# Performance work log

Hardware: AMD Instinct MI355X
Metric: run time of the kernel (lower is better)

The kernel has to match this reference:

```python
import jax, jax.numpy as jnp
import numpy as np

B, C, H, W = 256, 3, 224, 224
RETINA = 32
NUM_ZOOM = 3
SCALE = 2
HG, HL = 1024, 256  # num_hidden_glimpse, num_hidden_location
GDIM = NUM_ZOOM * C * RETINA * RETINA  # 9216


def setup_inputs() -> dict:
    key = jax.random.key(0)
    ks = jax.random.split(key, 12)
    images = jax.random.normal(ks[0], (B, C, H, W), dtype=jnp.float32)
    # locations in [-0.4, 0.4] so all multi-scale crops are in-bounds
    locations = (jax.random.uniform(ks[1], (B, 2), dtype=jnp.float32) * 2.0 - 1.0) * 0.4
    def lin(kw, kb, fan_in, fan_out):
        s = 1.0 / np.sqrt(fan_in)
        Wm = jax.random.uniform(kw, (fan_in, fan_out), jnp.float32, -s, s)
        bm = jax.random.uniform(kb, (fan_out,), jnp.float32, -s, s)
        return Wm, bm
    W1, b1 = lin(ks[2], ks[3], GDIM, HG)
    W2, b2 = lin(ks[4], ks[5], 2, HL)
    W3, b3 = lin(ks[6], ks[7], HG, HG + HL)
    W4, b4 = lin(ks[8], ks[9], HL, HG + HL)
    return {"images": images, "locations": locations,
            "W1": W1, "b1": b1, "W2": W2, "b2": b2,
            "W3": W3, "b3": b3, "W4": W4, "b4": b4}


def _foveate(images, locations):
    # images (B,C,H,W); locations (B,2) in [-1,1]
    denorm = (locations + 1.0) * 0.5 * W  # denormalized pixel coords (row, col)
    zoom_patches = []
    for i in range(NUM_ZOOM):
        half = int(RETINA * 0.5 * SCALE ** i)
        size = 2 * half
        def crop(img, loc):
            # int() truncation == floor for in-bounds (non-negative) offsets
            top = jnp.trunc(loc[0] - half).astype(jnp.int32)
            left = jnp.trunc(loc[1] - half).astype(jnp.int32)
            return jax.lax.dynamic_slice(img, (jnp.int32(0), top, left), (C, size, size))
        crops = jax.vmap(crop)(images, denorm)  # (B,C,size,size)
        resized = jax.image.resize(crops, (crops.shape[0], C, RETINA, RETINA),
                                   method="bilinear", antialias=False)
        zoom_patches.append(resized)
    g = jnp.stack(zoom_patches, axis=1)  # (B, Z, C, r, r)
    return g.reshape(g.shape[0], -1)  # (B, Z*C*r*r)


def reference(images, locations, W1, b1, W2, b2, W3, b3, W4, b4):
    g = _foveate(images, locations)
    hg = jax.nn.relu(jax.nn.relu(g @ W1 + b1) @ W3 + b3)
    hl = jax.nn.relu(jax.nn.relu(locations @ W2 + b2) @ W4 + b4)
    return jax.nn.relu(hg + hl)
```

## Files before the change

kernel.cpp:

```cpp
#include <hip/hip_runtime.h>

typedef __attribute__((ext_vector_type(8))) short short8;
typedef __attribute__((ext_vector_type(4))) float f32x4;

#define Bsz 256
#define Cch 3
#define Him 224
#define Wim 224
#define RET 32
#define HG 1024
#define HL 256
#define GDIM 9216
#define NOUT 1280

__device__ __forceinline__ unsigned short f2bf(float x) {
  unsigned u = __float_as_uint(x);
  unsigned r = (u + 0x7fffu + ((u >> 16) & 1u)) >> 16;
  return (unsigned short)r;
}
__device__ __forceinline__ float bf2f(unsigned short h) {
  return __uint_as_float((unsigned)h << 16);
}

__global__ __launch_bounds__(256) void foveate_kernel(
    const float* __restrict__ img, const float* __restrict__ loc,
    unsigned short* __restrict__ ghi, unsigned short* __restrict__ glo) {
  int idx = blockIdx.x * 256 + threadIdx.x;
  int b = idx / GDIM;
  int r = idx - b * GDIM;
  int z = r / (Cch * RET * RET);
  int r2 = r - z * (Cch * RET * RET);
  int c = r2 / (RET * RET);
  int p = r2 - c * (RET * RET);
  int i = p >> 5, j = p & 31;
  float dr = (loc[b * 2 + 0] + 1.f) * .5f * (float)Wim;
  float dc = (loc[b * 2 + 1] + 1.f) * .5f * (float)Wim;
  int half = 16 << z;
  int top = (int)truncf(dr - (float)half), left = (int)truncf(dc - (float)half);
  const float* base = img + ((long)b * Cch + c) * (Him * Wim);
  float v;
  if (z == 0) {
    v = base[(top + i) * Wim + left + j];
  } else {
    int rr = (z == 1) ? top + 2 * i : top + 4 * i + 1;
    int cc = (z == 1) ? left + 2 * j : left + 4 * j + 1;
    v = .25f * (base[rr * Wim + cc] + base[rr * Wim + cc + 1] +
                base[(rr + 1) * Wim + cc] + base[(rr + 1) * Wim + cc + 1]);
  }
  unsigned short h = f2bf(v);
  ghi[idx] = h;
  glo[idx] = f2bf(v - bf2f(h));
}

__global__ __launch_bounds__(256) void tconv_kernel(
    const float* __restrict__ in, unsigned short* __restrict__ oh,
    unsigned short* __restrict__ ol, int K, int N) {
  __shared__ float tile[32][33];
  int n0 = blockIdx.x * 32, k0 = blockIdx.y * 32;
  int r = threadIdx.x >> 3, c4 = (threadIdx.x & 7) * 4;
  float4 v = *(const float4*)(in + (long)(k0 + r) * N + n0 + c4);
  tile[r][c4 + 0] = v.x; tile[r][c4 + 1] = v.y;
  tile[r][c4 + 2] = v.z; tile[r][c4 + 3] = v.w;
  __syncthreads();
  float x0 = tile[c4 + 0][r], x1 = tile[c4 + 1][r];
  float x2 = tile[c4 + 2][r], x3 = tile[c4 + 3][r];
  unsigned short h0 = f2bf(x0), h1 = f2bf(x1), h2 = f2bf(x2), h3 = f2bf(x3);
  long o = (long)(n0 + r) * K + k0 + c4;
  *(ushort4*)(oh + o) = make_ushort4(h0, h1, h2, h3);
  *(ushort4*)(ol + o) = make_ushort4(f2bf(x0 - bf2f(h0)), f2bf(x1 - bf2f(h1)),
                                     f2bf(x2 - bf2f(h2)), f2bf(x3 - bf2f(h3)));
}

__device__ __forceinline__ void mfma_tile(
    const unsigned short* __restrict__ Ahi, const unsigned short* __restrict__ Alo, int lda,
    const unsigned short* __restrict__ Bhi, const unsigned short* __restrict__ Blo, int ldb,
    int m0, int n0, int kb, int iters, f32x4 acc[4][4], unsigned short* lds) {
  const int t = threadIdx.x;
  const int lane = t & 63;
  const int wm = (t >> 7) & 1, wn = (t >> 6) & 1;
  unsigned short* pAh = lds;
  unsigned short* pAl = lds + 4096;
  unsigned short* pBh = lds + 8192;
  unsigned short* pBl = lds + 12288;
  const int c0 = t, c1 = t + 256;
  const int r0 = c0 >> 2, ko0 = c0 & 3;
  const int r1 = c1 >> 2, ko1 = c1 & 3;
  const long a0 = (long)(m0 + r0) * lda + kb + ko0 * 8;
  const long a1 = (long)(m0 + r1) * lda + kb + ko1 * 8;
  const long b0 = (long)(n0 + r0) * ldb + kb + ko0 * 8;
  const long b1 = (long)(n0 + r1) * ldb + kb + ko1 * 8;
  const int d0 = ((r0 >> 4) * 64 + (r0 & 15) + ko0 * 16) * 8;
  const int d1 = ((r1 >> 4) * 64 + (r1 & 15) + ko1 * 16) * 8;

  for (int it = 0; it < iters; ++it) {
    const long ka = (long)it * 32;
    uint4 vah0 = *(const uint4*)(Ahi + a0 + ka);
    uint4 vah1 = *(const uint4*)(Ahi + a1 + ka);
    uint4 val0 = *(const uint4*)(Alo + a0 + ka);
    uint4 val1 = *(const uint4*)(Alo + a1 + ka);
    uint4 vbh0 = *(const uint4*)(Bhi + b0 + ka);
    uint4 vbh1 = *(const uint4*)(Bhi + b1 + ka);
    uint4 vbl0 = *(const uint4*)(Blo + b0 + ka);
    uint4 vbl1 = *(const uint4*)(Blo + b1 + ka);
    __syncthreads();
    *(uint4*)(pAh + d0) = vah0; *(uint4*)(pAh + d1) = vah1;
    *(uint4*)(pAl + d0) = val0; *(uint4*)(pAl + d1) = val1;
    *(uint4*)(pBh + d0) = vbh0; *(uint4*)(pBh + d1) = vbh1;
    *(uint4*)(pBl + d0) = vbl0; *(uint4*)(pBl + d1) = vbl1;
    __syncthreads();
    short8 ah[4], al[4], bh[4], bl[4];
#pragma unroll
    for (int f = 0; f < 4; ++f) {
      int ra = ((wm * 4 + f) * 64 + lane) * 8;
      int rb = ((wn * 4 + f) * 64 + lane) * 8;
      ah[f] = *(const short8*)(pAh + ra);
      al[f] = *(const short8*)(pAl + ra);
      bh[f] = *(const short8*)(pBh + rb);
      bl[f] = *(const short8*)(pBl + rb);
    }
#pragma unroll
    for (int mf = 0; mf < 4; ++mf)
#pragma unroll
      for (int nf = 0; nf < 4; ++nf) {
        acc[mf][nf] = __builtin_amdgcn_mfma_f32_16x16x32_bf16(ah[mf], bh[nf], acc[mf][nf], 0, 0, 0);
        acc[mf][nf] = __builtin_amdgcn_mfma_f32_16x16x32_bf16(ah[mf], bl[nf], acc[mf][nf], 0, 0, 0);
        acc[mf][nf] = __builtin_amdgcn_mfma_f32_16x16x32_bf16(al[mf], bh[nf], acc[mf][nf], 0, 0, 0);
      }
  }
}

__device__ __forceinline__ void epilogue(float* __restrict__ Pz, int ldp, int m0, int n0,
                                         f32x4 acc[4][4]) {
  const int t = threadIdx.x, lane = t & 63;
  const int wm = (t >> 7) & 1, wn = (t >> 6) & 1;
  const int rbase = (lane >> 4) * 4, col = lane & 15;
#pragma unroll
  for (int mf = 0; mf < 4; ++mf)
#pragma unroll
    for (int nf = 0; nf < 4; ++nf) {
      int row = m0 + wm * 64 + mf * 16 + rbase;
      int cc = n0 + wn * 64 + nf * 16 + col;
#pragma unroll
      for (int r = 0; r < 4; ++r)
        Pz[(long)(row + r) * ldp + cc] = acc[mf][nf][r];
    }
}

__global__ __launch_bounds__(256, 2) void gemm1_kernel(
    const unsigned short* __restrict__ ghi, const unsigned short* __restrict__ glo,
    const unsigned short* __restrict__ w1thi, const unsigned short* __restrict__ w1tlo,
    float* __restrict__ P) {
  __shared__ __align__(16) unsigned short lds[16384];
  f32x4 zz = {0.f, 0.f, 0.f, 0.f};
  f32x4 acc[4][4];
  for (int i = 0; i < 4; ++i) for (int j = 0; j < 4; ++j) acc[i][j] = zz;
  int n0 = blockIdx.x * 128, m0 = blockIdx.y * 128, z = blockIdx.z;
  mfma_tile(ghi, glo, GDIM, w1thi, w1tlo, GDIM, m0, n0, z * 288, 9, acc, lds);
  epilogue(P + (long)z * Bsz * HG, HG, m0, n0, acc);
}

__global__ __launch_bounds__(256, 2) void gemm2_kernel(
    const unsigned short* __restrict__ h1hi, const unsigned short* __restrict__ h1lo,
    const unsigned short* __restrict__ h2hi, const unsigned short* __restrict__ h2lo,
    const unsigned short* __restrict__ w3thi, const unsigned short* __restrict__ w3tlo,
    const unsigned short* __restrict__ w4thi, const unsigned short* __restrict__ w4tlo,
    float* __restrict__ P) {
  __shared__ __align__(16) unsigned short lds[16384];
  f32x4 zz = {0.f, 0.f, 0.f, 0.f};
  f32x4 acc[4][4];
  for (int i = 0; i < 4; ++i) for (int j = 0; j < 4; ++j) acc[i][j] = zz;
  int n0 = blockIdx.x * 128, m0 = blockIdx.y * 128, z = blockIdx.z;
  if (z < 8)
    mfma_tile(h1hi, h1lo, HG, w3thi, w3tlo, HG, m0, n0, z * 128, 4, acc, lds);
  else
    mfma_tile(h2hi, h2lo, HL, w4thi, w4tlo, HL, m0, n0, 0, 8, acc, lds);
  epilogue(P + (long)z * Bsz * NOUT, NOUT, m0, n0, acc);
}

__global__ __launch_bounds__(256) void reduce1_kernel(
    const float* __restrict__ P, const float* __restrict__ b1,
    unsigned short* __restrict__ h1hi, unsigned short* __restrict__ h1lo) {
  int i4 = (blockIdx.x * 256 + threadIdx.x) * 4;
  float4 s = *(const float4*)(P + i4);
  for (int z = 1; z < 32; ++z) {
    float4 p = *(const float4*)(P + (long)z * (Bsz * HG) + i4);
    s.x += p.x; s.y += p.y; s.z += p.z; s.w += p.w;
  }
  int n = i4 & (HG - 1);
  float4 bb = *(const float4*)(b1 + n);
  float v0 = fmaxf(s.x + bb.x, 0.f), v1 = fmaxf(s.y + bb.y, 0.f);
  float v2 = fmaxf(s.z + bb.z, 0.f), v3 = fmaxf(s.w + bb.w, 0.f);
  unsigned short h0 = f2bf(v0), h1 = f2bf(v1), h2 = f2bf(v2), h3 = f2bf(v3);
  *(ushort4*)(h1hi + i4) = make_ushort4(h0, h1, h2, h3);
  *(ushort4*)(h1lo + i4) = make_ushort4(f2bf(v0 - bf2f(h0)), f2bf(v1 - bf2f(h1)),
                                        f2bf(v2 - bf2f(h2)), f2bf(v3 - bf2f(h3)));
}

__global__ __launch_bounds__(256) void h2_kernel(
    const float* __restrict__ loc, const float* __restrict__ W2,
    const float* __restrict__ b2, unsigned short* __restrict__ h2hi,
    unsigned short* __restrict__ h2lo) {
  int b = blockIdx.x, n = threadIdx.x;
  float s = fmaf(loc[b * 2], W2[n], fmaf(loc[b * 2 + 1], W2[HL + n], b2[n]));
  s = fmaxf(s, 0.f);
  unsigned short h = f2bf(s);
  h2hi[b * HL + n] = h;
  h2lo[b * HL + n] = f2bf(s - bf2f(h));
}

__global__ __launch_bounds__(256) void reduce2_kernel(
    const float* __restrict__ P, const float* __restrict__ b3,
    const float* __restrict__ b4, float* __restrict__ out) {
  int i4 = (blockIdx.x * 256 + threadIdx.x) * 4;
  float4 a = *(const float4*)(P + i4);
  for (int z = 1; z < 8; ++z) {
    float4 p = *(const float4*)(P + (long)z * (Bsz * NOUT) + i4);
    a.x += p.x; a.y += p.y; a.z += p.z; a.w += p.w;
  }
  float4 c = *(const float4*)(P + 8L * (Bsz * NOUT) + i4);
  int n = i4 % NOUT;
  float4 b3v = *(const float4*)(b3 + n);
  float4 b4v = *(const float4*)(b4 + n);
  float4 o;
  o.x = fmaxf(fmaxf(a.x + b3v.x, 0.f) + fmaxf(c.x + b4v.x, 0.f), 0.f);
  o.y = fmaxf(fmaxf(a.y + b3v.y, 0.f) + fmaxf(c.y + b4v.y, 0.f), 0.f);
  o.z = fmaxf(fmaxf(a.z + b3v.z, 0.f) + fmaxf(c.z + b4v.z, 0.f), 0.f);
  o.w = fmaxf(fmaxf(a.w + b3v.w, 0.f) + fmaxf(c.w + b4v.w, 0.f), 0.f);
  *(float4*)(out + i4) = o;
}

extern "C" void kernel_launch(void* const* d_in, const int* in_sizes, int n_in,
                              void* d_out, int out_size, void* d_ws, size_t ws_size,
                              hipStream_t stream) {
  const float* images = (const float*)d_in[0];
  const float* locs = (const float*)d_in[1];
  const float* W1 = (const float*)d_in[2];
  const float* b1 = (const float*)d_in[3];
  const float* W2 = (const float*)d_in[4];
  const float* b2 = (const float*)d_in[5];
  const float* W3 = (const float*)d_in[6];
  const float* b3 = (const float*)d_in[7];
  const float* W4 = (const float*)d_in[8];
  const float* b4 = (const float*)d_in[9];
  float* out = (float*)d_out;

  unsigned short* ghi = (unsigned short*)d_ws;
  unsigned short* glo = ghi + (long)Bsz * GDIM;
  unsigned short* w1thi = glo + (long)Bsz * GDIM;
  unsigned short* w1tlo = w1thi + (long)GDIM * HG;
  unsigned short* w3thi = w1tlo + (long)GDIM * HG;
  unsigned short* w3tlo = w3thi + (long)HG * NOUT;
  unsigned short* w4thi = w3tlo + (long)HG * NOUT;
  unsigned short* w4tlo = w4thi + (long)HL * NOUT;
  unsigned short* h1hi = w4tlo + (long)HL * NOUT;
  unsigned short* h1lo = h1hi + (long)Bsz * HG;
  unsigned short* h2hi = h1lo + (long)Bsz * HG;
  unsigned short* h2lo = h2hi + (long)Bsz * HL;
  float* P1 = (float*)(h2lo + (long)Bsz * HL);
  float* P2 = P1;

  tconv_kernel<<<dim3(HG / 32, GDIM / 32), 256, 0, stream>>>(W1, w1thi, w1tlo, GDIM, HG);
  tconv_kernel<<<dim3(NOUT / 32, HG / 32), 256, 0, stream>>>(W3, w3thi, w3tlo, HG, NOUT);
  tconv_kernel<<<dim3(NOUT / 32, HL / 32), 256, 0, stream>>>(W4, w4thi, w4tlo, HL, NOUT);
  foveate_kernel<<<(Bsz * GDIM) / 256, 256, 0, stream>>>(images, locs, ghi, glo);
  gemm1_kernel<<<dim3(HG / 128, Bsz / 128, 32), 256, 0, stream>>>(ghi, glo, w1thi, w1tlo, P1);
  reduce1_kernel<<<(Bsz * HG) / 1024, 256, 0, stream>>>(P1, b1, h1hi, h1lo);
  h2_kernel<<<Bsz, HL, 0, stream>>>(locs, W2, b2, h2hi, h2lo);
  gemm2_kernel<<<dim3(NOUT / 128, Bsz / 128, 9), 256, 0, stream>>>(
      h1hi, h1lo, h2hi, h2lo, w3thi, w3tlo, w4thi, w4tlo, P2);
  reduce2_kernel<<<(Bsz * NOUT) / 1024, 256, 0, stream>>>(P2, b3, b4, out);
}
```

Baseline: 299.0 us.

## Split fp32 weights into bf16 hi/lo inside GEMMs instead of pre-transposing

Removes the three weight transpose/convert kernels and has the GEMMs load fp32 weights directly from row-major layout into shared memory, splitting them into bf16 hi/lo pairs on the fly. The MFMA tiles move from 16x16x32 to 32x32x16. The reduce1 and h2 kernels are merged into one launch. The W4 GEMM is split across two z-slices, with P2 placed separately from P1. This drops about 21M weight elements of conversion traffic per call. In exchange it adds per-K-step conversion ALU work and strided LDS reads of the fp32 B tile.

```diff
diff --git a/kernel.cpp b/kernel.cpp
--- a/kernel.cpp
+++ b/kernel.cpp
@@ -1,7 +1,7 @@
 #include <hip/hip_runtime.h>
 
 typedef __attribute__((ext_vector_type(8))) short short8;
-typedef __attribute__((ext_vector_type(4))) float f32x4;
+typedef __attribute__((ext_vector_type(16))) float f32x16;
 
 #define Bsz 256
 #define Cch 3
@@ -15,8 +15,7 @@
 
 __device__ __forceinline__ unsigned short f2bf(float x) {
   unsigned u = __float_as_uint(x);
-  unsigned r = (u + 0x7fffu + ((u >> 16) & 1u)) >> 16;
-  return (unsigned short)r;
+  return (unsigned short)((u + 0x7fffu + ((u >> 16) & 1u)) >> 16);
 }
 __device__ __forceinline__ float bf2f(unsigned short h) {
   return __uint_as_float((unsigned)h << 16);
@@ -52,160 +51,167 @@
   glo[idx] = f2bf(v - bf2f(h));
 }
 
-__global__ __launch_bounds__(256) void tconv_kernel(
-    const float* __restrict__ in, unsigned short* __restrict__ oh,
-    unsigned short* __restrict__ ol, int K, int N) {
-  __shared__ float tile[32][33];
-  int n0 = blockIdx.x * 32, k0 = blockIdx.y * 32;
-  int r = threadIdx.x >> 3, c4 = (threadIdx.x & 7) * 4;
-  float4 v = *(const float4*)(in + (long)(k0 + r) * N + n0 + c4);
-  tile[r][c4 + 0] = v.x; tile[r][c4 + 1] = v.y;
-  tile[r][c4 + 2] = v.z; tile[r][c4 + 3] = v.w;
-  __syncthreads();
-  float x0 = tile[c4 + 0][r], x1 = tile[c4 + 1][r];
-  float x2 = tile[c4 + 2][r], x3 = tile[c4 + 3][r];
-  unsigned short h0 = f2bf(x0), h1 = f2bf(x1), h2 = f2bf(x2), h3 = f2bf(x3);
-  long o = (long)(n0 + r) * K + k0 + c4;
-  *(ushort4*)(oh + o) = make_ushort4(h0, h1, h2, h3);
-  *(ushort4*)(ol + o) = make_ushort4(f2bf(x0 - bf2f(h0)), f2bf(x1 - bf2f(h1)),
-                                     f2bf(x2 - bf2f(h2)), f2bf(x3 - bf2f(h3)));
-}
-
-__device__ __forceinline__ void mfma_tile(
-    const unsigned short* __restrict__ Ahi, const unsigned short* __restrict__ Alo, int lda,
-    const unsigned short* __restrict__ Bhi, const unsigned short* __restrict__ Blo, int ldb,
-    int m0, int n0, int kb, int iters, f32x4 acc[4][4], unsigned short* lds) {
+__device__ __forceinline__ void gemm_block(
+    const unsigned short* __restrict__ Ahi, const unsigned short* __restrict__ Alo,
+    int lda, const float* __restrict__ Bf, int ldb,
+    int m0, int n0, int kb, int iters,
+    f32x16 acc[2][2], unsigned short* __restrict__ ldsA, float* __restrict__ ldsB) {
   const int t = threadIdx.x;
   const int lane = t & 63;
-  const int wm = (t >> 7) & 1, wn = (t >> 6) & 1;
-  unsigned short* pAh = lds;
-  unsigned short* pAl = lds + 4096;
-  unsigned short* pBh = lds + 8192;
-  unsigned short* pBl = lds + 12288;
-  const int c0 = t, c1 = t + 256;
-  const int r0 = c0 >> 2, ko0 = c0 & 3;
-  const int r1 = c1 >> 2, ko1 = c1 & 3;
-  const long a0 = (long)(m0 + r0) * lda + kb + ko0 * 8;
-  const long a1 = (long)(m0 + r1) * lda + kb + ko1 * 8;
-  const long b0 = (long)(n0 + r0) * ldb + kb + ko0 * 8;
-  const long b1 = (long)(n0 + r1) * ldb + kb + ko1 * 8;
-  const int d0 = ((r0 >> 4) * 64 + (r0 & 15) + ko0 * 16) * 8;
-  const int d1 = ((r1 >> 4) * 64 + (r1 & 15) + ko1 * 16) * 8;
+  const int wm = t >> 7, wn = (t >> 6) & 1;
+  const int l5 = lane & 31, lh = lane >> 5;
+
+  const unsigned short* aSrc[4];
+  const float* bSrc[4];
+  int aDst[4], bDst[4];
+#pragma unroll
+  for (int p = 0; p < 4; ++p) {
+    int s = p * 256 + t;
+    int m5 = s & 31, kseg = (s >> 5) & 3, mf = (s >> 7) & 3;
+    const unsigned short* base = (s >> 9) ? Alo : Ahi;
+    aSrc[p] = base + (long)(m0 + mf * 32 + m5) * lda + kb + kseg * 8;
+    aDst[p] = s * 8;
+    bSrc[p] = Bf + (long)(kb + (s & 1023) / 32) * ldb + n0 + (s & 31) * 4;
+    bDst[p] = ((s & 1023) >> 5) * 128 + (s & 31) * 4;
+  }
 
   for (int it = 0; it < iters; ++it) {
-    const long ka = (long)it * 32;
-    uint4 vah0 = *(const uint4*)(Ahi + a0 + ka);
-    uint4 vah1 = *(const uint4*)(Ahi + a1 + ka);
-    uint4 val0 = *(const uint4*)(Alo + a0 + ka);
-    uint4 val1 = *(const uint4*)(Alo + a1 + ka);
-    uint4 vbh0 = *(const uint4*)(Bhi + b0 + ka);
-    uint4 vbh1 = *(const uint4*)(Bhi + b1 + ka);
-    uint4 vbl0 = *(const uint4*)(Blo + b0 + ka);
-    uint4 vbl1 = *(const uint4*)(Blo + b1 + ka);
+    uint4 av[4];
+    float4 bv[4];
+#pragma unroll
+    for (int p = 0; p < 4; ++p) {
+      av[p] = *(const uint4*)(aSrc[p] + it * 32);
+      bv[p] = *(const float4*)(bSrc[p] + (long)it * 32 * ldb);
+    }
     __syncthreads();
-    *(uint4*)(pAh + d0) = vah0; *(uint4*)(pAh + d1) = vah1;
-    *(uint4*)(pAl + d0) = val0; *(uint4*)(pAl + d1) = val1;
-    *(uint4*)(pBh + d0) = vbh0; *(uint4*)(pBh + d1) = vbh1;
-    *(uint4*)(pBl + d0) = vbl0; *(uint4*)(pBl + d1) = vbl1;
+#pragma unroll
+    for (int p = 0; p < 4; ++p) {
+      *(uint4*)(ldsA + aDst[p]) = av[p];
+      *(float4*)(ldsB + bDst[p]) = bv[p];
+    }
     __syncthreads();
-    short8 ah[4], al[4], bh[4], bl[4];
-#pragma unroll
-    for (int f = 0; f < 4; ++f) {
-      int ra = ((wm * 4 + f) * 64 + lane) * 8;
-      int rb = ((wn * 4 + f) * 64 + lane) * 8;
-      ah[f] = *(const short8*)(pAh + ra);
-      al[f] = *(const short8*)(pAl + ra);
-      bh[f] = *(const short8*)(pBh + rb);
-      bl[f] = *(const short8*)(pBl + rb);
-    }
-#pragma unroll
-    for (int mf = 0; mf < 4; ++mf)
-#pragma unroll
-      for (int nf = 0; nf < 4; ++nf) {
-        acc[mf][nf] = __builtin_amdgcn_mfma_f32_16x16x32_bf16(ah[mf], bh[nf], acc[mf][nf], 0, 0, 0);
-        acc[mf][nf] = __builtin_amdgcn_mfma_f32_16x16x32_bf16(ah[mf], bl[nf], acc[mf][nf], 0, 0, 0);
-        acc[mf][nf] = __builtin_amdgcn_mfma_f32_16x16x32_bf16(al[mf], bh[nf], acc[mf][nf], 0, 0, 0);
+#pragma unroll
+    for (int ks = 0; ks < 2; ++ks) {
+      short8 ah[2], al[2], bh[2], bl[2];
+#pragma unroll
+      for (int mi = 0; mi < 2; ++mi) {
+        int mf = wm * 2 + mi;
+        int slot = mf * 128 + (ks * 2 + lh) * 32 + l5;
+        ah[mi] = *(const short8*)(ldsA + slot * 8);
+        al[mi] = *(const short8*)(ldsA + (slot + 512) * 8);
       }
-  }
-}
-
-__device__ __forceinline__ void epilogue(float* __restrict__ Pz, int ldp, int m0, int n0,
-                                         f32x4 acc[4][4]) {
+#pragma unroll
+      for (int ni = 0; ni < 2; ++ni) {
+        int n = wn * 64 + ni * 32 + l5;
+        int k0 = ks * 16 + lh * 8;
+        short8 hh, ll;
+#pragma unroll
+        for (int j = 0; j < 8; ++j) {
+          float v = ldsB[(k0 + j) * 128 + n];
+          unsigned short h = f2bf(v);
+          hh[j] = (short)h;
+          ll[j] = (short)f2bf(v - bf2f(h));
+        }
+        bh[ni] = hh;
+        bl[ni] = ll;
+      }
+#pragma unroll
+      for (int mi = 0; mi < 2; ++mi)
+#pragma unroll
+        for (int ni = 0; ni < 2; ++ni) {
+          acc[mi][ni] = __builtin_amdgcn_mfma_f32_32x32x16_bf16(ah[mi], bh[ni], acc[mi][ni], 0, 0, 0);
+          acc[mi][ni] = __builtin_amdgcn_mfma_f32_32x32x16_bf16(ah[mi], bl[ni], acc[mi][ni], 0, 0, 0);
+          acc[mi][ni] = __builtin_amdgcn_mfma_f32_32x32x16_bf16(al[mi], bh[ni], acc[mi][ni], 0, 0, 0);
+        }
+    }
+  }
+}
+
+__device__ __forceinline__ void epilogue(float* __restrict__ Pz, int ldp, int m0,
+                                         int n0, f32x16 acc[2][2]) {
   const int t = threadIdx.x, lane = t & 63;
-  const int wm = (t >> 7) & 1, wn = (t >> 6) & 1;
-  const int rbase = (lane >> 4) * 4, col = lane & 15;
-#pragma unroll
-  for (int mf = 0; mf < 4; ++mf)
-#pragma unroll
-    for (int nf = 0; nf < 4; ++nf) {
-      int row = m0 + wm * 64 + mf * 16 + rbase;
-      int cc = n0 + wn * 64 + nf * 16 + col;
-#pragma unroll
-      for (int r = 0; r < 4; ++r)
-        Pz[(long)(row + r) * ldp + cc] = acc[mf][nf][r];
+  const int wm = t >> 7, wn = (t >> 6) & 1;
+  const int l5 = lane & 31, lh = lane >> 5;
+#pragma unroll
+  for (int mi = 0; mi < 2; ++mi)
+#pragma unroll
+    for (int ni = 0; ni < 2; ++ni) {
+      int col = n0 + wn * 64 + ni * 32 + l5;
+      int rbase = m0 + wm * 64 + mi * 32 + 4 * lh;
+#pragma unroll
+      for (int r = 0; r < 16; ++r) {
+        int row = rbase + (r & 3) + 8 * (r >> 2);
+        Pz[(long)row * ldp + col] = acc[mi][ni][r];
+      }
     }
 }
 
 __global__ __launch_bounds__(256, 2) void gemm1_kernel(
     const unsigned short* __restrict__ ghi, const unsigned short* __restrict__ glo,
-    const unsigned short* __restrict__ w1thi, const unsigned short* __restrict__ w1tlo,
-    float* __restrict__ P) {
-  __shared__ __align__(16) unsigned short lds[16384];
-  f32x4 zz = {0.f, 0.f, 0.f, 0.f};
-  f32x4 acc[4][4];
-  for (int i = 0; i < 4; ++i) for (int j = 0; j < 4; ++j) acc[i][j] = zz;
+    const float* __restrict__ W1, float* __restrict__ P) {
+  __shared__ __align__(16) unsigned short ldsA[8192];
+  __shared__ __align__(16) float ldsB[4096];
+  f32x16 zz = {0, 0, 0, 0, 0, 0, 0, 0, 0, 0, 0, 0, 0, 0, 0, 0};
+  f32x16 acc[2][2] = {zz, zz, zz, zz};
   int n0 = blockIdx.x * 128, m0 = blockIdx.y * 128, z = blockIdx.z;
-  mfma_tile(ghi, glo, GDIM, w1thi, w1tlo, GDIM, m0, n0, z * 288, 9, acc, lds);
+  gemm_block(ghi, glo, GDIM, W1, HG, m0, n0, z * 288, 9, acc, ldsA, ldsB);
   epilogue(P + (long)z * Bsz * HG, HG, m0, n0, acc);
 }
 
 __global__ __launch_bounds__(256, 2) void gemm2_kernel(
     const unsigned short* __restrict__ h1hi, const unsigned short* __restrict__ h1lo,
     const unsigned short* __restrict__ h2hi, const unsigned short* __restrict__ h2lo,
-    const unsigned short* __restrict__ w3thi, const unsigned short* __restrict__ w3tlo,
-    const unsigned short* __restrict__ w4thi, const unsigned short* __restrict__ w4tlo,
+    const float* __restrict__ W3, const float* __restrict__ W4,
     float* __restrict__ P) {
-  __shared__ __align__(16) unsigned short lds[16384];
-  f32x4 zz = {0.f, 0.f, 0.f, 0.f};
-  f32x4 acc[4][4];
-  for (int i = 0; i < 4; ++i) for (int j = 0; j < 4; ++j) acc[i][j] = zz;
+  __shared__ __align__(16) unsigned short ldsA[8192];
+  __shared__ __align__(16) float ldsB[4096];
+  f32x16 zz = {0, 0, 0, 0, 0, 0, 0, 0, 0, 0, 0, 0, 0, 0, 0, 0};
+  f32x16 acc[2][2] = {zz, zz, zz, zz};
   int n0 = blockIdx.x * 128, m0 = blockIdx.y * 128, z = blockIdx.z;
   if (z < 8)
-    mfma_tile(h1hi, h1lo, HG, w3thi, w3tlo, HG, m0, n0, z * 128, 4, acc, lds);
+    gemm_block(h1hi, h1lo, HG, W3, NOUT, m0, n0, z * 128, 4, acc, ldsA, ldsB);
   else
-    mfma_tile(h2hi, h2lo, HL, w4thi, w4tlo, HL, m0, n0, 0, 8, acc, lds);
+    gemm_block(h2hi, h2lo, HL, W4, NOUT, m0, n0, (z - 8) * 128, 4, acc, ldsA, ldsB);
   epilogue(P + (long)z * Bsz * NOUT, NOUT, m0, n0, acc);
 }
 
-__global__ __launch_bounds__(256) void reduce1_kernel(
+__global__ __launch_bounds__(256) void reduce1_h2_kernel(
     const float* __restrict__ P, const float* __restrict__ b1,
-    unsigned short* __restrict__ h1hi, unsigned short* __restrict__ h1lo) {
-  int i4 = (blockIdx.x * 256 + threadIdx.x) * 4;
-  float4 s = *(const float4*)(P + i4);
-  for (int z = 1; z < 32; ++z) {
-    float4 p = *(const float4*)(P + (long)z * (Bsz * HG) + i4);
-    s.x += p.x; s.y += p.y; s.z += p.z; s.w += p.w;
-  }
-  int n = i4 & (HG - 1);
-  float4 bb = *(const float4*)(b1 + n);
-  float v0 = fmaxf(s.x + bb.x, 0.f), v1 = fmaxf(s.y + bb.y, 0.f);
-  float v2 = fmaxf(s.z + bb.z, 0.f), v3 = fmaxf(s.w + bb.w, 0.f);
-  unsigned short h0 = f2bf(v0), h1 = f2bf(v1), h2 = f2bf(v2), h3 = f2bf(v3);
-  *(ushort4*)(h1hi + i4) = make_ushort4(h0, h1, h2, h3);
-  *(ushort4*)(h1lo + i4) = make_ushort4(f2bf(v0 - bf2f(h0)), f2bf(v1 - bf2f(h1)),
-                                        f2bf(v2 - bf2f(h2)), f2bf(v3 - bf2f(h3)));
-}
-
-__global__ __launch_bounds__(256) void h2_kernel(
     const float* __restrict__ loc, const float* __restrict__ W2,
-    const float* __restrict__ b2, unsigned short* __restrict__ h2hi,
-    unsigned short* __restrict__ h2lo) {
-  int b = blockIdx.x, n = threadIdx.x;
-  float s = fmaf(loc[b * 2], W2[n], fmaf(loc[b * 2 + 1], W2[HL + n], b2[n]));
-  s = fmaxf(s, 0.f);
-  unsigned short h = f2bf(s);
-  h2hi[b * HL + n] = h;
-  h2lo[b * HL + n] = f2bf(s - bf2f(h));
+    const float* __restrict__ b2,
+    unsigned short* __restrict__ h1hi, unsigned short* __restrict__ h1lo,
+    unsigned short* __restrict__ h2hi, unsigned short* __restrict__ h2lo) {
+  if (blockIdx.x < 256) {
+    int i4 = (blockIdx.x * 256 + threadIdx.x) * 4;
+    float4 s = *(const float4*)(P + i4);
+    for (int z = 1; z < 32; ++z) {
+      float4 p = *(const float4*)(P + (long)z * (Bsz * HG) + i4);
+      s.x += p.x; s.y += p.y; s.z += p.z; s.w += p.w;
+    }
+    int n = i4 & (HG - 1);
+    float4 bb = *(const float4*)(b1 + n);
+    float v0 = fmaxf(s.x + bb.x, 0.f), v1 = fmaxf(s.y + bb.y, 0.f);
+    float v2 = fmaxf(s.z + bb.z, 0.f), v3 = fmaxf(s.w + bb.w, 0.f);
+    unsigned short h0 = f2bf(v0), h1 = f2bf(v1), h2 = f2bf(v2), h3 = f2bf(v3);
+    *(ushort4*)(h1hi + i4) = make_ushort4(h0, h1, h2, h3);
+    *(ushort4*)(h1lo + i4) = make_ushort4(f2bf(v0 - bf2f(h0)), f2bf(v1 - bf2f(h1)),
+                                          f2bf(v2 - bf2f(h2)), f2bf(v3 - bf2f(h3)));
+  } else {
+    int i4 = ((blockIdx.x - 256) * 256 + threadIdx.x) * 4;
+    int b = i4 >> 8, n = i4 & (HL - 1);
+    float l0 = loc[b * 2 + 0], l1 = loc[b * 2 + 1];
+    float4 w0 = *(const float4*)(W2 + n);
+    float4 w1 = *(const float4*)(W2 + HL + n);
+    float4 bb = *(const float4*)(b2 + n);
+    float v0 = fmaxf(fmaf(l0, w0.x, fmaf(l1, w1.x, bb.x)), 0.f);
+    float v1 = fmaxf(fmaf(l0, w0.y, fmaf(l1, w1.y, bb.y)), 0.f);
+    float v2 = fmaxf(fmaf(l0, w0.z, fmaf(l1, w1.z, bb.z)), 0.f);
+    float v3 = fmaxf(fmaf(l0, w0.w, fmaf(l1, w1.w, bb.w)), 0.f);
+    unsigned short h0 = f2bf(v0), h1 = f2bf(v1), h2 = f2bf(v2), h3 = f2bf(v3);
+    *(ushort4*)(h2hi + i4) = make_ushort4(h0, h1, h2, h3);
+    *(ushort4*)(h2lo + i4) = make_ushort4(f2bf(v0 - bf2f(h0)), f2bf(v1 - bf2f(h1)),
+                                          f2bf(v2 - bf2f(h2)), f2bf(v3 - bf2f(h3)));
+  }
 }
 
 __global__ __launch_bounds__(256) void reduce2_kernel(
@@ -217,15 +223,16 @@
     float4 p = *(const float4*)(P + (long)z * (Bsz * NOUT) + i4);
     a.x += p.x; a.y += p.y; a.z += p.z; a.w += p.w;
   }
-  float4 c = *(const float4*)(P + 8L * (Bsz * NOUT) + i4);
+  float4 c8 = *(const float4*)(P + 8L * (Bsz * NOUT) + i4);
+  float4 c9 = *(const float4*)(P + 9L * (Bsz * NOUT) + i4);
   int n = i4 % NOUT;
   float4 b3v = *(const float4*)(b3 + n);
   float4 b4v = *(const float4*)(b4 + n);
   float4 o;
-  o.x = fmaxf(fmaxf(a.x + b3v.x, 0.f) + fmaxf(c.x + b4v.x, 0.f), 0.f);
-  o.y = fmaxf(fmaxf(a.y + b3v.y, 0.f) + fmaxf(c.y + b4v.y, 0.f), 0.f);
-  o.z = fmaxf(fmaxf(a.z + b3v.z, 0.f) + fmaxf(c.z + b4v.z, 0.f), 0.f);
-  o.w = fmaxf(fmaxf(a.w + b3v.w, 0.f) + fmaxf(c.w + b4v.w, 0.f), 0.f);
+  o.x = fmaxf(fmaxf(a.x + b3v.x, 0.f) + fmaxf(c8.x + c9.x + b4v.x, 0.f), 0.f);
+  o.y = fmaxf(fmaxf(a.y + b3v.y, 0.f) + fmaxf(c8.y + c9.y + b4v.y, 0.f), 0.f);
+  o.z = fmaxf(fmaxf(a.z + b3v.z, 0.f) + fmaxf(c8.z + c9.z + b4v.z, 0.f), 0.f);
+  o.w = fmaxf(fmaxf(a.w + b3v.w, 0.f) + fmaxf(c8.w + c9.w + b4v.w, 0.f), 0.f);
   *(float4*)(out + i4) = o;
 }
 
@@ -246,27 +253,17 @@
 
   unsigned short* ghi = (unsigned short*)d_ws;
   unsigned short* glo = ghi + (long)Bsz * GDIM;
-  unsigned short* w1thi = glo + (long)Bsz * GDIM;
-  unsigned short* w1tlo = w1thi + (long)GDIM * HG;
-  unsigned short* w3thi = w1tlo + (long)GDIM * HG;
-  unsigned short* w3tlo = w3thi + (long)HG * NOUT;
-  unsigned short* w4thi = w3tlo + (long)HG * NOUT;
-  unsigned short* w4tlo = w4thi + (long)HL * NOUT;
-  unsigned short* h1hi = w4tlo + (long)HL * NOUT;
+  unsigned short* h1hi = glo + (long)Bsz * GDIM;
   unsigned short* h1lo = h1hi + (long)Bsz * HG;
   unsigned short* h2hi = h1lo + (long)Bsz * HG;
   unsigned short* h2lo = h2hi + (long)Bsz * HL;
   float* P1 = (float*)(h2lo + (long)Bsz * HL);
-  float* P2 = P1;
-
-  tconv_kernel<<<dim3(HG / 32, GDIM / 32), 256, 0, stream>>>(W1, w1thi, w1tlo, GDIM, HG);
-  tconv_kernel<<<dim3(NOUT / 32, HG / 32), 256, 0, stream>>>(W3, w3thi, w3tlo, HG, NOUT);
-  tconv_kernel<<<dim3(NOUT / 32, HL / 32), 256, 0, stream>>>(W4, w4thi, w4tlo, HL, NOUT);
+  float* P2 = P1 + 32L * Bsz * HG;
+
   foveate_kernel<<<(Bsz * GDIM) / 256, 256, 0, stream>>>(images, locs, ghi, glo);
-  gemm1_kernel<<<dim3(HG / 128, Bsz / 128, 32), 256, 0, stream>>>(ghi, glo, w1thi, w1tlo, P1);
-  reduce1_kernel<<<(Bsz * HG) / 1024, 256, 0, stream>>>(P1, b1, h1hi, h1lo);
-  h2_kernel<<<Bsz, HL, 0, stream>>>(locs, W2, b2, h2hi, h2lo);
-  gemm2_kernel<<<dim3(NOUT / 128, Bsz / 128, 9), 256, 0, stream>>>(
-      h1hi, h1lo, h2hi, h2lo, w3thi, w3tlo, w4thi, w4tlo, P2);
+  gemm1_kernel<<<dim3(HG / 128, Bsz / 128, 32), 256, 0, stream>>>(ghi, glo, W1, P1);
+  reduce1_h2_kernel<<<320, 256, 0, stream>>>(P1, b1, locs, W2, b2, h1hi, h1lo, h2hi, h2lo);
+  gemm2_kernel<<<dim3(NOUT / 128, Bsz / 128, 10), 256, 0, stream>>>(
+      h1hi, h1lo, h2hi, h2lo, W3, W4, P2);
   reduce2_kernel<<<(Bsz * NOUT) / 1024, 256, 0, stream>>>(P2, b3, b4, out);
 }
```

After: 343.8 us. 15.0% more time.
